# Kernel optimization log

Measured on AMD Instinct MI355X. Metric: run time of the kernel, lower is better.

The kernel has to match this reference:

```python
import jax, jax.numpy as jnp
import numpy as np

def setup_inputs() -> dict:
    key = jax.random.key(0)
    kq, kk, kv = jax.random.split(key, 3)
    S, D = 4096, 512
    q = jax.random.normal(kq, (S, D), dtype=jnp.float32)
    k = jax.random.normal(kk, (S, D), dtype=jnp.float32)
    v = jax.random.normal(kv, (S, D), dtype=jnp.float32)
    return {"q": q, "k": k, "v": v}

def reference(q, k, v):
    # scaled dot-product attention, unmasked (mask_future=False path)
    d = q.shape[-1]
    scores = jnp.einsum('sd,td->st', q, k) / jnp.sqrt(jnp.asarray(d, q.dtype))
    attn = jax.nn.softmax(scores, axis=-1)
    return jnp.einsum('st,td->sd', attn, v)
```

## Files before the change

### kernel.cpp

```cpp
#include <hip/hip_runtime.h>
#include <hip/hip_bf16.h>

#define SEQ 4096
#define DIM 512
#define SCALE 0.044194173824159216f

#define SPLITS 4
#define BQ 64
#define KVBLK 64
#define KEYS_PER_SPLIT (SEQ / SPLITS)
#define ITERS (KEYS_PER_SPLIT / KVBLK)
#define THR_DEFER 8.0f

typedef __attribute__((ext_vector_type(8))) short short8;
typedef __attribute__((ext_vector_type(4))) float f32x4;
typedef __attribute__((ext_vector_type(16))) float f32x16;

__device__ __forceinline__ short f2bf(float f) {
  union { float f; unsigned u; } c; c.f = f;
  unsigned u = c.u;
  return (short)((u + 0x7FFFu + ((u >> 16) & 1u)) >> 16);
}

__device__ __forceinline__ short8 pack8(float4 a, float4 b) {
  short8 r;
  r[0] = f2bf(a.x); r[1] = f2bf(a.y); r[2] = f2bf(a.z); r[3] = f2bf(a.w);
  r[4] = f2bf(b.x); r[5] = f2bf(b.y); r[6] = f2bf(b.z); r[7] = f2bf(b.w);
  return r;
}

__device__ __forceinline__ ushort4 pack4(float a, float b, float c, float d) {
  ushort4 r;
  r.x = (unsigned short)f2bf(a); r.y = (unsigned short)f2bf(b);
  r.z = (unsigned short)f2bf(c); r.w = (unsigned short)f2bf(d);
  return r;
}

__device__ __forceinline__ void gload16(const void* g, void* l) {
  __builtin_amdgcn_global_load_lds(
      (const __attribute__((address_space(1))) unsigned int*)g,
      (__attribute__((address_space(3))) unsigned int*)l, 16, 0, 0);
}

__global__ void cvt_bf16(const float* __restrict__ in, ushort* __restrict__ ob, int n8) {
  int i = blockIdx.x * blockDim.x + threadIdx.x;
  if (i >= n8) return;
  const float4* p = (const float4*)(in + (size_t)i * 8);
  short8 v = pack8(p[0], p[1]);
  *(short8*)(ob + (size_t)i * 8) = v;
}

__global__ void transpose_bf16(const float* __restrict__ v, ushort* __restrict__ vt) {
  __shared__ float t[64][65];
  const int bs = blockIdx.x % (SEQ / 64);
  const int bd = blockIdx.x / (SEQ / 64);
  const int s0 = bs * 64, d0 = bd * 64;
  const int tid = threadIdx.x;
#pragma unroll
  for (int k = 0; k < 16; ++k) {
    int idx = k * 256 + tid;
    int r = idx >> 6, c = idx & 63;
    t[r][c] = v[(size_t)(s0 + r) * DIM + d0 + c];
  }
  __syncthreads();
#pragma unroll
  for (int k = 0; k < 16; ++k) {
    int idx = k * 256 + tid;
    int dr = idx >> 6, sc = idx & 63;
    vt[(size_t)(d0 + dr) * SEQ + s0 + sc] = (ushort)f2bf(t[sc][dr]);
  }
}

__global__ __launch_bounds__(512, 2) void attn_split(
    const float* __restrict__ q, const ushort* __restrict__ kbf,
    const ushort* __restrict__ vt, float* __restrict__ opart,
    float* __restrict__ ml) {
  __shared__ __align__(16) ushort kt[KVBLK * DIM];
  __shared__ __align__(16) ushort vtt[DIM * KVBLK];
  __shared__ __align__(16) ushort p_lds[BQ * KVBLK];
  __shared__ float mx_st[2][BQ];
  __shared__ float osc_st[BQ];
  __shared__ float l_st[2][BQ];
  __shared__ int   flag_st[4];

  const int tid  = threadIdx.x;
  const int lane = tid & 63;
  const int w    = tid >> 6;
  const int lr   = lane & 15;
  const int lg   = lane >> 4;
  const int l31  = lane & 31;
  const int hi   = lane >> 5;
  const int sp   = blockIdx.x & (SPLITS - 1);
  const int qb   = blockIdx.x >> 2;
  const int rg   = w & 3;
  const int kh   = w >> 2;
  const int rg_pv = w & 1;
  const int cg    = w >> 1;
  const int qrow0 = qb * BQ;
  const int kbase = sp * KEYS_PER_SPLIT;

  short8 qf[16];
  {
    const float* qp = q + (size_t)(qrow0 + rg * 16 + lr) * DIM + lg * 8;
#pragma unroll
    for (int c = 0; c < 16; ++c)
      qf[c] = pack8(*(const float4*)(qp + c * 32), *(const float4*)(qp + c * 32 + 4));
  }
  f32x16 oacc[4] = {};
  float m_reg = -INFINITY, l_reg = 0.f;

  auto stageK = [&](int kb) {
#pragma unroll
    for (int i = 0; i < 8; ++i) {
      int r = w * 8 + i;
      const ushort* src = kbf + (size_t)(kb + r) * DIM + ((lane ^ (r & 31)) * 8);
      gload16(src, &kt[r * DIM]);
    }
  };
  auto stageV = [&](int kb) {
#pragma unroll
    for (int j = 0; j < 8; ++j) {
      int r0 = w * 64 + j * 8;
      int rr = r0 + (lane >> 3);
      const ushort* src = vt + (size_t)rr * SEQ + kb + (((lane & 7) ^ (rr & 7)) * 8);
      gload16(src, &vtt[r0 * KVBLK]);
    }
  };

  stageK(kbase);

#pragma unroll 1
  for (int it = 0; it < ITERS; ++it) {
    const int kb = kbase + it * KVBLK;

    asm volatile("s_waitcnt vmcnt(0)" ::: "memory");
    __builtin_amdgcn_s_barrier();

    stageV(kb);

    f32x4 s0 = {}, s1 = {};
    {
      const int kr0 = kh * 32 + lr;
      const int kr1 = kr0 + 16;
      const char* kb0 = (const char*)kt + kr0 * 1024;
      const char* kb1 = (const char*)kt + kr1 * 1024;
      const int sw0 = kr0 & 31, sw1 = kr1 & 31;
      __builtin_amdgcn_s_setprio(1);
#pragma unroll
      for (int c = 0; c < 16; ++c) {
        short8 k0 = *(const short8*)(kb0 + (((c * 4 + lg) ^ sw0) << 4));
        short8 k1 = *(const short8*)(kb1 + (((c * 4 + lg) ^ sw1) << 4));
        s0 = __builtin_amdgcn_mfma_f32_16x16x32_bf16(k0, qf[c], s0, 0, 0, 0);
        s1 = __builtin_amdgcn_mfma_f32_16x16x32_bf16(k1, qf[c], s1, 0, 0, 0);
      }
      __builtin_amdgcn_s_setprio(0);
    }

    float sc0[4], sc1[4];
#pragma unroll
    for (int r = 0; r < 4; ++r) { sc0[r] = s0[r] * SCALE; sc1[r] = s1[r] * SCALE; }
    float tmax = fmaxf(fmaxf(fmaxf(sc0[0], sc0[1]), fmaxf(sc0[2], sc0[3])),
                       fmaxf(fmaxf(sc1[0], sc1[1]), fmaxf(sc1[2], sc1[3])));
    tmax = fmaxf(tmax, __shfl_xor(tmax, 16));
    tmax = fmaxf(tmax, __shfl_xor(tmax, 32));
    if (lane < 16) mx_st[kh][rg * 16 + lane] = tmax;

    asm volatile("s_waitcnt lgkmcnt(0)" ::: "memory");
    __builtin_amdgcn_s_barrier();

    if (it + 1 < ITERS) stageK(kb + KVBLK);

    {
      const int row = rg * 16 + lr;
      float tmax64 = fmaxf(mx_st[0][row], mx_st[1][row]);
      bool resc = tmax64 > m_reg + THR_DEFER;
      float mnew = resc ? tmax64 : m_reg;
      float osc = __expf(m_reg - mnew);
      unsigned long long bl = __ballot(resc);
      if (kh == 0 && lane == 0) flag_st[rg] = (bl != 0ull) ? 1 : 0;
      if (kh == 0 && lane < 16) osc_st[row] = osc;
      m_reg = mnew;
      l_reg *= osc;
      float p0[4], p1[4];
#pragma unroll
      for (int r = 0; r < 4; ++r) {
        p0[r] = __expf(sc0[r] - m_reg);
        p1[r] = __expf(sc1[r] - m_reg);
      }
      float ps = ((p0[0] + p0[1]) + (p0[2] + p0[3])) +
                 ((p1[0] + p1[1]) + (p1[2] + p1[3]));
      ps += __shfl_xor(ps, 16);
      ps += __shfl_xor(ps, 32);
      l_reg += ps;
      char* pb = (char*)p_lds + row * 128;
      const int sw = (row & 7) << 4;
      const int off = kh * 64 + lg * 8;
      *(ushort4*)(pb + (off ^ sw))        = pack4(p0[0], p0[1], p0[2], p0[3]);
      *(ushort4*)(pb + ((off + 32) ^ sw)) = pack4(p1[0], p1[1], p1[2], p1[3]);
    }

    if (it + 1 < ITERS) {
      asm volatile("s_waitcnt vmcnt(8)" ::: "memory");
    } else {
      asm volatile("s_waitcnt vmcnt(0)" ::: "memory");
    }
    asm volatile("s_waitcnt lgkmcnt(0)" ::: "memory");
    __builtin_amdgcn_s_barrier();

    {
      if (flag_st[rg_pv * 2] | flag_st[rg_pv * 2 + 1]) {
        float ov[16];
#pragma unroll
        for (int r = 0; r < 16; ++r)
          ov[r] = osc_st[rg_pv * 32 + (r & 3) + 8 * (r >> 2) + 4 * hi];
#pragma unroll
        for (int t = 0; t < 4; ++t)
#pragma unroll
          for (int r = 0; r < 16; ++r) oacc[t][r] *= ov[r];
      }
      const int arow = rg_pv * 32 + l31;
      const char* prow = (const char*)p_lds + arow * 128;
      const int psw = (arow & 7) << 4;
      __builtin_amdgcn_s_setprio(1);
#pragma unroll
      for (int c = 0; c < 4; ++c) {
        short8 pa = *(const short8*)(prow + ((c * 32 + hi * 16) ^ psw));
#pragma unroll
        for (int t = 0; t < 4; ++t) {
          int vrow = cg * 128 + t * 32 + l31;
          short8 vf = *(const short8*)((const char*)vtt + vrow * 128 +
                                       ((c * 32 + hi * 16) ^ ((vrow & 7) << 4)));
          oacc[t] = __builtin_amdgcn_mfma_f32_32x32x16_bf16(pa, vf, oacc[t], 0, 0, 0);
        }
      }
      __builtin_amdgcn_s_setprio(0);
    }
  }

  if (lane < 16) {
    l_st[kh][rg * 16 + lane] = l_reg;
    if (kh == 0) mx_st[0][rg * 16 + lane] = m_reg;
  }
  __syncthreads();
  {
    float* op = opart + ((size_t)sp * SEQ + qrow0 + rg_pv * 32) * DIM + cg * 128;
#pragma unroll
    for (int t = 0; t < 4; ++t)
#pragma unroll
      for (int r = 0; r < 16; ++r) {
        int crow = (r & 3) + 8 * (r >> 2) + 4 * hi;
        op[(size_t)crow * DIM + t * 32 + l31] = oacc[t][r];
      }
  }
  if (tid < BQ) {
    size_t base = ((size_t)sp * SEQ + qrow0 + tid) * 2;
    ml[base]     = mx_st[0][tid];
    ml[base + 1] = l_st[0][tid] + l_st[1][tid];
  }
}

__global__ void combine(const float* __restrict__ opart, const float* __restrict__ ml,
                        float* __restrict__ out) {
  int gid = blockIdx.x * 256 + threadIdx.x;
  int row = gid >> 7;
  int dv  = (gid & 127) * 4;
  float m[SPLITS], l[SPLITS], wgt[SPLITS];
  float M = -INFINITY;
#pragma unroll
  for (int i = 0; i < SPLITS; ++i) {
    m[i] = ml[((size_t)i * SEQ + row) * 2];
    l[i] = ml[((size_t)i * SEQ + row) * 2 + 1];
    M = fmaxf(M, m[i]);
  }
  float L = 0.f;
#pragma unroll
  for (int i = 0; i < SPLITS; ++i) { wgt[i] = __expf(m[i] - M); L += l[i] * wgt[i]; }
  float inv = 1.f / L;
  float4 acc = {0.f, 0.f, 0.f, 0.f};
#pragma unroll
  for (int i = 0; i < SPLITS; ++i) {
    float4 o = *(const float4*)(opart + ((size_t)i * SEQ + row) * DIM + dv);
    acc.x += o.x * wgt[i]; acc.y += o.y * wgt[i];
    acc.z += o.z * wgt[i]; acc.w += o.w * wgt[i];
  }
  acc.x *= inv; acc.y *= inv; acc.z *= inv; acc.w *= inv;
  *(float4*)(out + (size_t)row * DIM + dv) = acc;
}

__global__ __launch_bounds__(512) void attn_fused_fb(
    const float* __restrict__ q, const float* __restrict__ k,
    const float* __restrict__ v, float* __restrict__ out) {
  __shared__ float s_lds[16][128];
  __shared__ __align__(16) unsigned short p_lds[16 * 128];
  __shared__ float m_st[16], l_st[16], osc_st[16];
  const int tid = threadIdx.x, lane = tid & 63, w = tid >> 6;
  const int lr = lane & 15, lg = lane >> 4, qb = blockIdx.x * 16;
  if (tid < 16) { m_st[tid] = -INFINITY; l_st[tid] = 0.f; }
  short8 qf[16];
  {
    const float* qp = q + (size_t)(qb + lr) * DIM + lg * 8;
#pragma unroll
    for (int c = 0; c < 16; ++c)
      qf[c] = pack8(*(const float4*)(qp + c * 32), *(const float4*)(qp + c * 32 + 4));
  }
  f32x4 oacc[4] = {};
  __syncthreads();
  for (int it = 0; it < SEQ / 128; ++it) {
    const int kb = it * 128;
    {
      const float* kp = k + (size_t)(kb + w * 16 + lr) * DIM + lg * 8;
      f32x4 sacc = {};
#pragma unroll
      for (int c = 0; c < 16; ++c) {
        short8 kf = pack8(*(const float4*)(kp + c * 32), *(const float4*)(kp + c * 32 + 4));
        sacc = __builtin_amdgcn_mfma_f32_16x16x32_bf16(qf[c], kf, sacc, 0, 0, 0);
      }
#pragma unroll
      for (int r = 0; r < 4; ++r) s_lds[lg * 4 + r][w * 16 + lr] = sacc[r] * SCALE;
    }
    __syncthreads();
    {
      const int srow = tid >> 5, sj = tid & 31;
      float4 sv = *(const float4*)&s_lds[srow][sj * 4];
      float tmax = fmaxf(fmaxf(sv.x, sv.y), fmaxf(sv.z, sv.w));
#pragma unroll
      for (int m = 16; m >= 1; m >>= 1) tmax = fmaxf(tmax, __shfl_xor(tmax, m));
      float mold = m_st[srow], mnew = fmaxf(mold, tmax);
      float p0 = __expf(sv.x - mnew), p1 = __expf(sv.y - mnew);
      float p2 = __expf(sv.z - mnew), p3 = __expf(sv.w - mnew);
      float psum = (p0 + p1) + (p2 + p3);
#pragma unroll
      for (int m = 16; m >= 1; m >>= 1) psum += __shfl_xor(psum, m);
      if (sj == 0) {
        float sc = __expf(mold - mnew);
        l_st[srow] = l_st[srow] * sc + psum; m_st[srow] = mnew; osc_st[srow] = sc;
      }
      ushort4 pb;
      pb.x = (unsigned short)f2bf(p0); pb.y = (unsigned short)f2bf(p1);
      pb.z = (unsigned short)f2bf(p2); pb.w = (unsigned short)f2bf(p3);
      int lin = srow * 256 + sj * 8;
      *(ushort4*)((char*)p_lds + (lin ^ ((srow & 7) << 4))) = pb;
    }
    __syncthreads();
    {
      float osc[4];
#pragma unroll
      for (int r = 0; r < 4; ++r) osc[r] = osc_st[lg * 4 + r];
#pragma unroll
      for (int ct = 0; ct < 4; ++ct)
#pragma unroll
        for (int r = 0; r < 4; ++r) oacc[ct][r] *= osc[r];
#pragma unroll
      for (int kc = 0; kc < 4; ++kc) {
        int lin = lr * 256 + (kc * 32 + 8 * lg) * 2;
        short8 pf = *(const short8*)((const char*)p_lds + (lin ^ ((lr & 7) << 4)));
        const float* vp0 = v + (size_t)(kb + kc * 32 + 8 * lg) * DIM + w * 64 + lr;
#pragma unroll
        for (int ct = 0; ct < 4; ++ct) {
          const float* vp = vp0 + ct * 16;
          short8 vf;
#pragma unroll
          for (int jj = 0; jj < 8; ++jj) vf[jj] = f2bf(vp[(size_t)jj * DIM]);
          oacc[ct] = __builtin_amdgcn_mfma_f32_16x16x32_bf16(pf, vf, oacc[ct], 0, 0, 0);
        }
      }
    }
    __syncthreads();
  }
  {
    float linv[4];
#pragma unroll
    for (int r = 0; r < 4; ++r) linv[r] = 1.f / l_st[lg * 4 + r];
#pragma unroll
    for (int ct = 0; ct < 4; ++ct)
#pragma unroll
      for (int r = 0; r < 4; ++r)
        out[(size_t)(qb + lg * 4 + r) * DIM + w * 64 + ct * 16 + lr] =
            oacc[ct][r] * linv[r];
  }
}

extern "C" void kernel_launch(void* const* d_in, const int* in_sizes, int n_in,
                              void* d_out, int out_size, void* d_ws, size_t ws_size,
                              hipStream_t stream) {
  (void)in_sizes; (void)n_in; (void)out_size;
  const float* q = (const float*)d_in[0];
  const float* k = (const float*)d_in[1];
  const float* v = (const float*)d_in[2];
  float* out = (float*)d_out;

  const size_t kbf_elems = (size_t)SEQ * DIM;
  const size_t vt_elems  = (size_t)DIM * SEQ;
  const size_t op_elems  = (size_t)SPLITS * SEQ * DIM;
  const size_t ml_elems  = (size_t)SPLITS * SEQ * 2;
  const size_t need = kbf_elems * 2 + vt_elems * 2 + op_elems * 4 + ml_elems * 4;

  if (ws_size >= need) {
    ushort* kbf  = (ushort*)d_ws;
    ushort* vtb  = kbf + kbf_elems;
    float* opart = (float*)(vtb + vt_elems);
    float* ml    = opart + op_elems;

    cvt_bf16<<<(SEQ * DIM / 8 + 255) / 256, 256, 0, stream>>>(k, kbf, SEQ * DIM / 8);
    transpose_bf16<<<(SEQ / 64) * (DIM / 64), 256, 0, stream>>>(v, vtb);
    attn_split<<<(SEQ / BQ) * SPLITS, 512, 0, stream>>>(q, kbf, vtb, opart, ml);
    combine<<<(SEQ * DIM / 4) / 256, 256, 0, stream>>>(opart, ml, out);
  } else {
    attn_fused_fb<<<SEQ / 16, 512, 0, stream>>>(q, k, v, out);
  }
}
```

Baseline: 87.04 us.

## Merge K-convert and V-transpose kernels; store split partials in bf16

Merges the K bf16 conversion and the V transpose into one launch by partitioning the block index, which removes one kernel launch. The per-split partial outputs are now written as bf16 instead of fp32, which halves the partial-output traffic written by attn_split and read by combine. Combine now handles 8 elements per thread. The cost is an extra rounding of unnormalized partial outputs to bf16 before the weighted merge, which reduces accuracy.

```diff
diff --git a/kernel.cpp b/kernel.cpp
--- a/kernel.cpp
+++ b/kernel.cpp
@@ -22,6 +22,12 @@
   return (short)((u + 0x7FFFu + ((u >> 16) & 1u)) >> 16);
 }
 
+__device__ __forceinline__ float bf2f(unsigned short b) {
+  union { unsigned u; float f; } c;
+  c.u = ((unsigned)b) << 16;
+  return c.f;
+}
+
 __device__ __forceinline__ short8 pack8(float4 a, float4 b) {
   short8 r;
   r[0] = f2bf(a.x); r[1] = f2bf(a.y); r[2] = f2bf(a.z); r[3] = f2bf(a.w);
@@ -42,30 +48,31 @@
       (__attribute__((address_space(3))) unsigned int*)l, 16, 0, 0);
 }
 
-__global__ void cvt_bf16(const float* __restrict__ in, ushort* __restrict__ ob, int n8) {
-  int i = blockIdx.x * blockDim.x + threadIdx.x;
-  if (i >= n8) return;
-  const float4* p = (const float4*)(in + (size_t)i * 8);
-  short8 v = pack8(p[0], p[1]);
-  *(short8*)(ob + (size_t)i * 8) = v;
-}
-
-__global__ void transpose_bf16(const float* __restrict__ v, ushort* __restrict__ vt) {
+__global__ void prep_fused(const float* __restrict__ k, ushort* __restrict__ kbf,
+                           const float* __restrict__ v, ushort* __restrict__ vt) {
   __shared__ float t[64][65];
-  const int bs = blockIdx.x % (SEQ / 64);
-  const int bd = blockIdx.x / (SEQ / 64);
+  const int tid = threadIdx.x;
+  if (blockIdx.x < 1024) {
+    int i = blockIdx.x * 256 + tid;
+    const float4* p = (const float4*)(k + (size_t)i * 8);
+    short8 o = pack8(p[0], p[1]);
+    *(short8*)(kbf + (size_t)i * 8) = o;
+    return;
+  }
+  const int bid = blockIdx.x - 1024;
+  const int bs = bid % (SEQ / 64);
+  const int bd = bid / (SEQ / 64);
   const int s0 = bs * 64, d0 = bd * 64;
-  const int tid = threadIdx.x;
-#pragma unroll
-  for (int k = 0; k < 16; ++k) {
-    int idx = k * 256 + tid;
+#pragma unroll
+  for (int kk = 0; kk < 16; ++kk) {
+    int idx = kk * 256 + tid;
     int r = idx >> 6, c = idx & 63;
     t[r][c] = v[(size_t)(s0 + r) * DIM + d0 + c];
   }
   __syncthreads();
 #pragma unroll
-  for (int k = 0; k < 16; ++k) {
-    int idx = k * 256 + tid;
+  for (int kk = 0; kk < 16; ++kk) {
+    int idx = kk * 256 + tid;
     int dr = idx >> 6, sc = idx & 63;
     vt[(size_t)(d0 + dr) * SEQ + s0 + sc] = (ushort)f2bf(t[sc][dr]);
   }
@@ -73,7 +80,7 @@
 
 __global__ __launch_bounds__(512, 2) void attn_split(
     const float* __restrict__ q, const ushort* __restrict__ kbf,
-    const ushort* __restrict__ vt, float* __restrict__ opart,
+    const ushort* __restrict__ vt, ushort* __restrict__ opart,
     float* __restrict__ ml) {
   __shared__ __align__(16) ushort kt[KVBLK * DIM];
   __shared__ __align__(16) ushort vtt[DIM * KVBLK];
@@ -243,13 +250,13 @@
   }
   __syncthreads();
   {
-    float* op = opart + ((size_t)sp * SEQ + qrow0 + rg_pv * 32) * DIM + cg * 128;
+    ushort* op = opart + ((size_t)sp * SEQ + qrow0 + rg_pv * 32) * DIM + cg * 128;
 #pragma unroll
     for (int t = 0; t < 4; ++t)
 #pragma unroll
       for (int r = 0; r < 16; ++r) {
         int crow = (r & 3) + 8 * (r >> 2) + 4 * hi;
-        op[(size_t)crow * DIM + t * 32 + l31] = oacc[t][r];
+        op[(size_t)crow * DIM + t * 32 + l31] = (ushort)f2bf(oacc[t][r]);
       }
   }
   if (tid < BQ) {
@@ -259,11 +266,11 @@
   }
 }
 
-__global__ void combine(const float* __restrict__ opart, const float* __restrict__ ml,
+__global__ void combine(const ushort* __restrict__ opart, const float* __restrict__ ml,
                         float* __restrict__ out) {
   int gid = blockIdx.x * 256 + threadIdx.x;
-  int row = gid >> 7;
-  int dv  = (gid & 127) * 4;
+  int row = gid >> 6;
+  int dv  = (gid & 63) * 8;
   float m[SPLITS], l[SPLITS], wgt[SPLITS];
   float M = -INFINITY;
 #pragma unroll
@@ -276,15 +283,18 @@
 #pragma unroll
   for (int i = 0; i < SPLITS; ++i) { wgt[i] = __expf(m[i] - M); L += l[i] * wgt[i]; }
   float inv = 1.f / L;
-  float4 acc = {0.f, 0.f, 0.f, 0.f};
+  float acc[8] = {};
 #pragma unroll
   for (int i = 0; i < SPLITS; ++i) {
-    float4 o = *(const float4*)(opart + ((size_t)i * SEQ + row) * DIM + dv);
-    acc.x += o.x * wgt[i]; acc.y += o.y * wgt[i];
-    acc.z += o.z * wgt[i]; acc.w += o.w * wgt[i];
-  }
-  acc.x *= inv; acc.y *= inv; acc.z *= inv; acc.w *= inv;
-  *(float4*)(out + (size_t)row * DIM + dv) = acc;
+    short8 o = *(const short8*)(opart + ((size_t)i * SEQ + row) * DIM + dv);
+#pragma unroll
+    for (int j = 0; j < 8; ++j) acc[j] += bf2f((unsigned short)o[j]) * wgt[i];
+  }
+  float4 r0, r1;
+  r0.x = acc[0] * inv; r0.y = acc[1] * inv; r0.z = acc[2] * inv; r0.w = acc[3] * inv;
+  r1.x = acc[4] * inv; r1.y = acc[5] * inv; r1.z = acc[6] * inv; r1.w = acc[7] * inv;
+  *(float4*)(out + (size_t)row * DIM + dv)     = r0;
+  *(float4*)(out + (size_t)row * DIM + dv + 4) = r1;
 }
 
 __global__ __launch_bounds__(512) void attn_fused_fb(
@@ -393,18 +403,17 @@
   const size_t vt_elems  = (size_t)DIM * SEQ;
   const size_t op_elems  = (size_t)SPLITS * SEQ * DIM;
   const size_t ml_elems  = (size_t)SPLITS * SEQ * 2;
-  const size_t need = kbf_elems * 2 + vt_elems * 2 + op_elems * 4 + ml_elems * 4;
+  const size_t need = kbf_elems * 2 + vt_elems * 2 + op_elems * 2 + ml_elems * 4;
 
   if (ws_size >= need) {
     ushort* kbf  = (ushort*)d_ws;
     ushort* vtb  = kbf + kbf_elems;
-    float* opart = (float*)(vtb + vt_elems);
-    float* ml    = opart + op_elems;
-
-    cvt_bf16<<<(SEQ * DIM / 8 + 255) / 256, 256, 0, stream>>>(k, kbf, SEQ * DIM / 8);
-    transpose_bf16<<<(SEQ / 64) * (DIM / 64), 256, 0, stream>>>(v, vtb);
+    ushort* opart = vtb + vt_elems;
+    float* ml    = (float*)(opart + op_elems);
+
+    prep_fused<<<1024 + (SEQ / 64) * (DIM / 64), 256, 0, stream>>>(k, kbf, v, vtb);
     attn_split<<<(SEQ / BQ) * SPLITS, 512, 0, stream>>>(q, kbf, vtb, opart, ml);
-    combine<<<(SEQ * DIM / 4) / 256, 256, 0, stream>>>(opart, ml, out);
+    combine<<<(SEQ * DIM / 8) / 256, 256, 0, stream>>>(opart, ml, out);
   } else {
     attn_fused_fb<<<SEQ / 16, 512, 0, stream>>>(q, k, v, out);
   }
```

Result: faster. 79.70 us (-8.4%).
